# Optimization experiments

Hardware: AMD Instinct MI355X
Metric: run time of the kernel (lower is better)

The kernel has to match this reference:

```python
import jax, jax.numpy as jnp
import numpy as np

KEY_DIM = 512
VALUE_DIM = 128
CAPACITY = 500000
N_RETRIEVE = 16
LN_EPS = 1e-5
NORM_EPS = 1e-12


def _l2norm(x, axis=-1):
    # F.normalize: x / max(||x||, eps)
    n = jnp.sqrt(jnp.sum(x * x, axis=axis, keepdims=True))
    return x / jnp.maximum(n, NORM_EPS)


def setup_inputs() -> dict:
    key = jax.random.key(0)
    ks = jax.random.split(key, 5)
    s = 1.0 / np.sqrt(KEY_DIM)
    return {
        "query": jax.random.normal(ks[0], (1, KEY_DIM), jnp.float32),
        "W1": jax.random.normal(ks[1], (KEY_DIM, KEY_DIM), jnp.float32) * s,
        "b1": jnp.zeros((KEY_DIM,), jnp.float32),
        "W2": jax.random.normal(ks[2], (KEY_DIM, KEY_DIM), jnp.float32) * s,
        "b2": jnp.zeros((KEY_DIM,), jnp.float32),
        "gamma": jnp.ones((KEY_DIM,), jnp.float32),
        "beta": jnp.zeros((KEY_DIM,), jnp.float32),
        "keys": jax.random.normal(ks[3], (CAPACITY, KEY_DIM), jnp.float32),
        "values": jax.random.normal(ks[4], (CAPACITY, VALUE_DIM), jnp.float32),
    }


def reference(query, W1, b1, W2, b2, gamma, beta, keys, values):
    # read path detaches the query before projecting
    q = jax.lax.stop_gradient(query)                      # [1, D]
    h = jax.nn.silu(q @ W1.T + b1) @ W2.T + b2            # key_proj
    mu = jnp.mean(h, axis=-1, keepdims=True)
    var = jnp.var(h, axis=-1, keepdims=True)              # biased, like torch LN
    ln = (h - mu) / jnp.sqrt(var + LN_EPS) * gamma + beta
    qn = _l2norm(ln)[0]                                   # [D]
    kn = _l2norm(keys, axis=-1)                           # [N, D]
    sim = kn @ qn                                         # [N] cosine similarity
    top_sim, top_idx = jax.lax.top_k(sim, N_RETRIEVE)     # [k]
    attn = jax.nn.softmax(top_sim, axis=0)                # [k]
    vals = values[top_idx]                                # [k, V] gather
    out = attn @ vals                                     # [V] weighted sum
    return out
```

## Files before the change

### kernel.cpp

```cpp
#include <hip/hip_runtime.h>
#include <hip/hip_bf16.h>
#include <float.h>
#include <math.h>

#define KEY_DIM   512
#define VALUE_DIM 128
#define CAPACITY  500000
#define NRET      16

#define NBLKD     512
#define NBLKV     256
#define NBLKT     (NBLKD + NBLKV)
#define NSD       70
#define NDROWS    (NBLKD * NSD * 8)
#define ROFF      NDROWS
#define NVROWS    (CAPACITY - NDROWS)
#define VSWEEP    (NBLKV * 4 * 4)
#define RING      3

#define AS3 __attribute__((address_space(3)))
#define AS1 __attribute__((address_space(1)))

__device__ __forceinline__ float wave_sum(float x) {
#pragma unroll
    for (int s = 32; s > 0; s >>= 1) x += __shfl_xor(x, s);
    return x;
}

template <bool SILU>
__global__ __launch_bounds__(256) void matvec512(
        const float* __restrict__ W, const float* __restrict__ x,
        const float* __restrict__ b, float* __restrict__ y) {
    const int wid  = threadIdx.x >> 6;
    const int lane = threadIdx.x & 63;
    const int r = blockIdx.x * 4 + wid;

    const float4* Wr = (const float4*)(W + (size_t)r * KEY_DIM);
    const float4* xv = (const float4*)x;

    float4 w0 = Wr[lane], w1 = Wr[lane + 64];
    float4 x0 = xv[lane], x1 = xv[lane + 64];

    float dot = w0.x * x0.x + w0.y * x0.y + w0.z * x0.z + w0.w * x0.w
              + w1.x * x1.x + w1.y * x1.y + w1.z * x1.z + w1.w * x1.w;
    dot = wave_sum(dot);

    if (lane == 0) {
        float v = dot + b[r];
        if (SILU) v = v / (1.0f + expf(-v));
        y[r] = v;
    }
}

__global__ __launch_bounds__(512) void ln_l2norm(
        const float* __restrict__ h, const float* __restrict__ gamma,
        const float* __restrict__ beta, float* __restrict__ qn) {
    __shared__ float s1[8], s2[8];
    const int t = threadIdx.x;
    const int wid = t >> 6, lane = t & 63;

    float x = h[t];
    float a = x, bb = x * x;
#pragma unroll
    for (int s = 32; s > 0; s >>= 1) { a += __shfl_xor(a, s); bb += __shfl_xor(bb, s); }
    if (lane == 0) { s1[wid] = a; s2[wid] = bb; }
    __syncthreads();

    float suma = 0.f, sumb = 0.f;
#pragma unroll
    for (int i = 0; i < 8; ++i) { suma += s1[i]; sumb += s2[i]; }
    float mu  = suma * (1.0f / KEY_DIM);
    float var = sumb * (1.0f / KEY_DIM) - mu * mu;
    float ln  = (x - mu) / sqrtf(var + 1e-5f) * gamma[t] + beta[t];

    float c = wave_sum(ln * ln);
    __syncthreads();
    if (lane == 0) s1[wid] = c;
    __syncthreads();
    float ss = 0.f;
#pragma unroll
    for (int i = 0; i < 8; ++i) ss += s1[i];
    float n = fmaxf(sqrtf(ss), 1e-12f);
    qn[t] = ln / n;
}

__global__ __launch_bounds__(256) void sim_hybrid(
        const float* __restrict__ keys, const float* __restrict__ qn,
        float* __restrict__ cand_v, int* __restrict__ cand_i) {
    __shared__ float kl[RING][8][KEY_DIM];
    __shared__ float bv[64];
    __shared__ int   bi[64];

    const int tid  = threadIdx.x;
    const int w    = tid >> 6;
    const int lane = tid & 63;
    const int bid  = blockIdx.x;
    const int r3   = bid % 3;

    float v[16]; int id[16];
#pragma unroll
    for (int j = 0; j < 16; ++j) { v[j] = -FLT_MAX; id[j] = 0x7fffffff; }

    if (r3 < 2) {
        const int d    = (bid / 3) * 2 + r3;
        const int m    = lane & 31;
        const int rsel = lane >> 5;
        const int s0   = (d * 7919) % NSD;

        float4 qr[4];
        {
            const float4* q4 = (const float4*)qn;
#pragma unroll
            for (int j = 0; j < 4; ++j) qr[j] = q4[4 * m + j];
        }
        int srcoff0, srcoff1;
        {
            int p0 = lane,      g0 = p0 >> 2, sl0 = p0 & 3;
            int p1 = 64 + lane, g1 = p1 >> 2, sl1 = p1 & 3;
            srcoff0 = (4 * g0 + ((sl0 - (g0 >> 1)) & 3)) * 16;
            srcoff1 = (4 * g1 + ((sl1 - (g1 >> 1)) & 3)) * 16;
        }
        int roff[4];
#pragma unroll
        for (int j = 0; j < 4; ++j) roff[j] = (4 * m + ((j + (m >> 1)) & 3)) * 16;

        auto stage = [&](int G, int slot) {
#pragma unroll
            for (int i = 0; i < 4; ++i) {
                const int rl = 2 * w + (i >> 1);
                const int h  = i & 1;
                const char* gp = (const char*)(keys + ((size_t)G * 8 + rl) * KEY_DIM)
                                 + (h ? srcoff1 : srcoff0);
                float* lp = &kl[slot][rl][h * 256];
                __builtin_amdgcn_global_load_lds((const AS1 float*)gp, (AS3 float*)lp,
                                                 16, 0, 0);
            }
        };
        auto compute = [&](int G, int slot) {
            const char* rowbase = (const char*)&kl[slot][2 * w + rsel][0];
            float dot = 0.f, ss = 0.f;
#pragma unroll
            for (int j = 0; j < 4; ++j) {
                float4 k = *(const float4*)(rowbase + roff[j]);
                float4 q = qr[j];
                dot += k.x * q.x + k.y * q.y + k.z * q.z + k.w * q.w;
                ss  += k.x * k.x + k.y * k.y + k.z * k.z + k.w * k.w;
            }
#pragma unroll
            for (int s = 16; s > 0; s >>= 1) {
                dot += __shfl_xor(dot, s);
                ss  += __shfl_xor(ss, s);
            }
            float sim = dot / fmaxf(sqrtf(ss), 1e-12f);
#pragma unroll
            for (int q = 0; q < 2; ++q) {
                float sq = __shfl(sim, q * 32);
                if (sq > v[15]) {
                    float cv = sq; int ci = G * 8 + 2 * w + q;
#pragma unroll
                    for (int jj = 0; jj < 16; ++jj) {
                        if (cv > v[jj]) {
                            float tv = v[jj]; int ti = id[jj];
                            v[jj] = cv; id[jj] = ci; cv = tv; ci = ti;
                        }
                    }
                }
            }
        };

        {
            int se = s0;
            stage(d + se * NBLKD, 0);
            se = (se + 1 >= NSD) ? 0 : se + 1;
            stage(d + se * NBLKD, 1);
        }
        int scur = s0;
        int spre = s0 + 2; if (spre >= NSD) spre -= NSD;

#pragma unroll 1
        for (int s = 0; s < NSD; ++s) {
            stage(d + spre * NBLKD, (s + 2) % 3);
            spre = (spre + 1 >= NSD) ? 0 : spre + 1;
            asm volatile("s_waitcnt vmcnt(8)" ::: "memory");
            __builtin_amdgcn_sched_barrier(0);
            compute(d + scur * NBLKD, s % 3);
            __builtin_amdgcn_sched_barrier(0);
            scur = (scur + 1 >= NSD) ? 0 : scur + 1;
        }
        asm volatile("s_waitcnt vmcnt(0)" ::: "memory");
    } else {
        const int gw = (bid / 3) * 4 + w;
        const float4* q4 = (const float4*)qn;
        float4 q0 = q4[lane], q1 = q4[lane + 64];

#pragma unroll 1
        for (int base = gw * 4; base < NVROWS; base += VSWEEP) {
            float4 ka[4], kb[4];
#pragma unroll
            for (int j = 0; j < 4; ++j) {
                const float4* kp = (const float4*)(keys + (size_t)(ROFF + base + j) * KEY_DIM);
                ka[j] = kp[lane];
                kb[j] = kp[lane + 64];
            }
            float dot[4], ss[4];
#pragma unroll
            for (int j = 0; j < 4; ++j) {
                dot[j] = ka[j].x * q0.x + ka[j].y * q0.y + ka[j].z * q0.z + ka[j].w * q0.w
                       + kb[j].x * q1.x + kb[j].y * q1.y + kb[j].z * q1.z + kb[j].w * q1.w;
                ss[j]  = ka[j].x * ka[j].x + ka[j].y * ka[j].y + ka[j].z * ka[j].z + ka[j].w * ka[j].w
                       + kb[j].x * kb[j].x + kb[j].y * kb[j].y + kb[j].z * kb[j].z + kb[j].w * kb[j].w;
            }
#pragma unroll
            for (int s = 32; s > 0; s >>= 1) {
#pragma unroll
                for (int j = 0; j < 4; ++j) {
                    dot[j] += __shfl_xor(dot[j], s);
                    ss[j]  += __shfl_xor(ss[j], s);
                }
            }
#pragma unroll
            for (int j = 0; j < 4; ++j) {
                float sim = dot[j] / fmaxf(sqrtf(ss[j]), 1e-12f);
                if (sim > v[15]) {
                    float cv = sim; int ci = ROFF + base + j;
#pragma unroll
                    for (int jj = 0; jj < 16; ++jj) {
                        if (cv > v[jj]) {
                            float tv = v[jj]; int ti = id[jj];
                            v[jj] = cv; id[jj] = ci; cv = tv; ci = ti;
                        }
                    }
                }
            }
        }
    }

    if (lane == 0) {
#pragma unroll
        for (int j = 0; j < 16; ++j) { bv[w * 16 + j] = v[j]; bi[w * 16 + j] = id[j]; }
    }
    __syncthreads();
    if (w == 0) {
        const int cidx = (r3 < 2) ? ((bid / 3) * 2 + r3) : (NBLKD + bid / 3);
        float lv = bv[lane]; int li = bi[lane];
        for (int rr = 0; rr < NRET; ++rr) {
            float mv = lv; int mi = li;
#pragma unroll
            for (int s = 32; s > 0; s >>= 1) {
                float ov = __shfl_xor(mv, s); int oi = __shfl_xor(mi, s);
                if (ov > mv || (ov == mv && oi < mi)) { mv = ov; mi = oi; }
            }
            if (lane == 0) {
                cand_v[cidx * NRET + rr] = mv;
                cand_i[cidx * NRET + rr] = mi;
            }
            if (lv == mv && li == mi) { lv = -FLT_MAX; li = 0x7fffffff; }
        }
    }
}

__global__ __launch_bounds__(256) void merge_out(
        const float* __restrict__ cand_v, const int* __restrict__ cand_i,
        const float* __restrict__ values, float* __restrict__ out) {
    const int tid  = threadIdx.x;
    const int wid  = tid >> 6;
    const int lane = tid & 63;
    const int M4 = (NBLKT * NRET) / 4;

    float v[16]; int id[16];
#pragma unroll
    for (int j = 0; j < 16; ++j) { v[j] = -FLT_MAX; id[j] = 0x7fffffff; }

    const float4* cv4 = (const float4*)cand_v;
    const int4*   ci4 = (const int4*)cand_i;
    for (int c = tid; c < M4; c += 256) {
        float4 cv = cv4[c]; int4 ci = ci4[c];
        float cvs[4] = {cv.x, cv.y, cv.z, cv.w};
        int   cis[4] = {ci.x, ci.y, ci.z, ci.w};
#pragma unroll
        for (int u = 0; u < 4; ++u) {
            float cu = cvs[u]; int iu = cis[u];
            if (cu > v[15]) {
#pragma unroll
                for (int j = 0; j < 16; ++j) {
                    if (cu > v[j]) {
                        float tv = v[j]; int ti = id[j];
                        v[j] = cu; id[j] = iu; cu = tv; iu = ti;
                    }
                }
            }
        }
    }

    __shared__ float sv[64];
    __shared__ int   si[64];
    for (int rr = 0; rr < NRET; ++rr) {
        float mv = v[0]; int mi = id[0];
#pragma unroll
        for (int s = 32; s > 0; s >>= 1) {
            float ov = __shfl_xor(mv, s); int oi = __shfl_xor(mi, s);
            if (ov > mv || (ov == mv && oi < mi)) { mv = ov; mi = oi; }
        }
        if (v[0] == mv && id[0] == mi) {
#pragma unroll
            for (int j = 0; j < 15; ++j) { v[j] = v[j + 1]; id[j] = id[j + 1]; }
            v[15] = -FLT_MAX; id[15] = 0x7fffffff;
        }
        if (lane == 0) { sv[wid * 16 + rr] = mv; si[wid * 16 + rr] = mi; }
    }
    __syncthreads();

    if (wid == 0) {
        float lv = sv[lane]; int li = si[lane];
        float sel_v = -FLT_MAX; int sel_i = 0;
        for (int rr = 0; rr < NRET; ++rr) {
            float mv = lv; int mi = li;
#pragma unroll
            for (int s = 32; s > 0; s >>= 1) {
                float ov = __shfl_xor(mv, s); int oi = __shfl_xor(mi, s);
                if (ov > mv || (ov == mv && oi < mi)) { mv = ov; mi = oi; }
            }
            if (lv == mv && li == mi) { lv = -FLT_MAX; li = 0x7fffffff; }
            if (lane == rr) { sel_v = mv; sel_i = mi; }
        }

        float m0 = __shfl(sel_v, 0);
        float e = (lane < NRET) ? expf(sel_v - m0) : 0.0f;
        float denom = wave_sum(e);

        float acc0 = 0.f, acc1 = 0.f;
        for (int rr = 0; rr < NRET; ++rr) {
            float ar = __shfl(e, rr) / denom;
            int   ir = __shfl(sel_i, rr);
            const float* vr = values + (size_t)ir * VALUE_DIM;
            acc0 += ar * vr[lane];
            acc1 += ar * vr[lane + 64];
        }
        out[lane]      = acc0;
        out[lane + 64] = acc1;
    }
}

extern "C" void kernel_launch(void* const* d_in, const int* in_sizes, int n_in,
                              void* d_out, int out_size, void* d_ws, size_t ws_size,
                              hipStream_t stream) {
    const float* query  = (const float*)d_in[0];
    const float* W1     = (const float*)d_in[1];
    const float* b1     = (const float*)d_in[2];
    const float* W2     = (const float*)d_in[3];
    const float* b2     = (const float*)d_in[4];
    const float* gamma  = (const float*)d_in[5];
    const float* beta   = (const float*)d_in[6];
    const float* keys   = (const float*)d_in[7];
    const float* values = (const float*)d_in[8];
    float* out = (float*)d_out;

    float* ws = (float*)d_ws;
    float* h1     = ws;
    float* h2     = ws + 512;
    float* qn     = ws + 1024;
    float* cand_v = ws + 2048;
    int*   cand_i = (int*)(ws + 2048 + NBLKT * NRET);

    matvec512<true ><<<128, 256, 0, stream>>>(W1, query, b1, h1);
    matvec512<false><<<128, 256, 0, stream>>>(W2, h1, b2, h2);
    ln_l2norm<<<1, 512, 0, stream>>>(h2, gamma, beta, qn);
    sim_hybrid<<<NBLKT, 256, 0, stream>>>(keys, qn, cand_v, cand_i);
    merge_out<<<1, 256, 0, stream>>>(cand_v, cand_i, values, out);
}
```

Measured before the change: 313.1 us.

## Split DMA and direct-load work inside each block instead of across blocks

Replaces the block-level split with a split inside each block: every block now runs three waves on the LDS-DMA path and one wave on direct vector loads. The LDS-DMA path stages 6 rows per step and grows its ring from 3 to 4 slots, so three stages stay in flight. The row split is rebalanced to about 400k rows on the DMA path and the rest on direct loads. This aims to balance memory traffic across CUs and deepen prefetch. The risk is that a block now finishes only when its slowest wave does, so a mismatch between the two paths leaves waves idle.

```diff
diff --git a/kernel.cpp b/kernel.cpp
--- a/kernel.cpp
+++ b/kernel.cpp
@@ -8,15 +8,12 @@
 #define CAPACITY  500000
 #define NRET      16
 
-#define NBLKD     512
-#define NBLKV     256
-#define NBLKT     (NBLKD + NBLKV)
-#define NSD       70
-#define NDROWS    (NBLKD * NSD * 8)
-#define ROFF      NDROWS
-#define NVROWS    (CAPACITY - NDROWS)
-#define VSWEEP    (NBLKV * 4 * 4)
-#define RING      3
+#define NBLKS     768
+#define RING      4
+#define NSD       87
+#define DROWS     (NBLKS * 6 * NSD)
+#define VOFF      DROWS
+#define VSWEEP    (NBLKS * 4)
 
 #define AS3 __attribute__((address_space(3)))
 #define AS1 __attribute__((address_space(1)))
@@ -84,10 +81,10 @@
     qn[t] = ln / n;
 }
 
-__global__ __launch_bounds__(256) void sim_hybrid(
+__global__ __launch_bounds__(256) void sim_split(
         const float* __restrict__ keys, const float* __restrict__ qn,
         float* __restrict__ cand_v, int* __restrict__ cand_i) {
-    __shared__ float kl[RING][8][KEY_DIM];
+    __shared__ float kl[RING][6][KEY_DIM];
     __shared__ float bv[64];
     __shared__ int   bi[64];
 
@@ -95,17 +92,15 @@
     const int w    = tid >> 6;
     const int lane = tid & 63;
     const int bid  = blockIdx.x;
-    const int r3   = bid % 3;
 
     float v[16]; int id[16];
 #pragma unroll
     for (int j = 0; j < 16; ++j) { v[j] = -FLT_MAX; id[j] = 0x7fffffff; }
 
-    if (r3 < 2) {
-        const int d    = (bid / 3) * 2 + r3;
+    if (w < 3) {
         const int m    = lane & 31;
         const int rsel = lane >> 5;
-        const int s0   = (d * 7919) % NSD;
+        const int s0   = (bid * 7919) % NSD;
 
         float4 qr[4];
         {
@@ -124,19 +119,19 @@
 #pragma unroll
         for (int j = 0; j < 4; ++j) roff[j] = (4 * m + ((j + (m >> 1)) & 3)) * 16;
 
-        auto stage = [&](int G, int slot) {
+        auto stage = [&](int T, int slot) {
 #pragma unroll
             for (int i = 0; i < 4; ++i) {
                 const int rl = 2 * w + (i >> 1);
                 const int h  = i & 1;
-                const char* gp = (const char*)(keys + ((size_t)G * 8 + rl) * KEY_DIM)
+                const char* gp = (const char*)(keys + ((size_t)T * 6 + rl) * KEY_DIM)
                                  + (h ? srcoff1 : srcoff0);
                 float* lp = &kl[slot][rl][h * 256];
                 __builtin_amdgcn_global_load_lds((const AS1 float*)gp, (AS3 float*)lp,
                                                  16, 0, 0);
             }
         };
-        auto compute = [&](int G, int slot) {
+        auto compute = [&](int T, int slot) {
             const char* rowbase = (const char*)&kl[slot][2 * w + rsel][0];
             float dot = 0.f, ss = 0.f;
 #pragma unroll
@@ -153,10 +148,10 @@
             }
             float sim = dot / fmaxf(sqrtf(ss), 1e-12f);
 #pragma unroll
-            for (int q = 0; q < 2; ++q) {
-                float sq = __shfl(sim, q * 32);
+            for (int qq = 0; qq < 2; ++qq) {
+                float sq = __shfl(sim, qq * 32);
                 if (sq > v[15]) {
-                    float cv = sq; int ci = G * 8 + 2 * w + q;
+                    float cv = sq; int ci = T * 6 + 2 * w + qq;
 #pragma unroll
                     for (int jj = 0; jj < 16; ++jj) {
                         if (cv > v[jj]) {
@@ -170,35 +165,36 @@
 
         {
             int se = s0;
-            stage(d + se * NBLKD, 0);
+            stage(bid + se * NBLKS, 0);
             se = (se + 1 >= NSD) ? 0 : se + 1;
-            stage(d + se * NBLKD, 1);
+            stage(bid + se * NBLKS, 1);
+            se = (se + 1 >= NSD) ? 0 : se + 1;
+            stage(bid + se * NBLKS, 2);
         }
         int scur = s0;
-        int spre = s0 + 2; if (spre >= NSD) spre -= NSD;
+        int spre = s0 + 3; if (spre >= NSD) spre -= NSD;
 
 #pragma unroll 1
         for (int s = 0; s < NSD; ++s) {
-            stage(d + spre * NBLKD, (s + 2) % 3);
+            stage(bid + spre * NBLKS, (s + 3) & 3);
             spre = (spre + 1 >= NSD) ? 0 : spre + 1;
-            asm volatile("s_waitcnt vmcnt(8)" ::: "memory");
+            asm volatile("s_waitcnt vmcnt(12)" ::: "memory");
             __builtin_amdgcn_sched_barrier(0);
-            compute(d + scur * NBLKD, s % 3);
+            compute(bid + scur * NBLKS, s & 3);
             __builtin_amdgcn_sched_barrier(0);
             scur = (scur + 1 >= NSD) ? 0 : scur + 1;
         }
         asm volatile("s_waitcnt vmcnt(0)" ::: "memory");
     } else {
-        const int gw = (bid / 3) * 4 + w;
         const float4* q4 = (const float4*)qn;
         float4 q0 = q4[lane], q1 = q4[lane + 64];
 
 #pragma unroll 1
-        for (int base = gw * 4; base < NVROWS; base += VSWEEP) {
+        for (int base = VOFF + bid * 4; base < CAPACITY; base += VSWEEP) {
             float4 ka[4], kb[4];
 #pragma unroll
             for (int j = 0; j < 4; ++j) {
-                const float4* kp = (const float4*)(keys + (size_t)(ROFF + base + j) * KEY_DIM);
+                const float4* kp = (const float4*)(keys + (size_t)(base + j) * KEY_DIM);
                 ka[j] = kp[lane];
                 kb[j] = kp[lane + 64];
             }
@@ -222,7 +218,7 @@
             for (int j = 0; j < 4; ++j) {
                 float sim = dot[j] / fmaxf(sqrtf(ss[j]), 1e-12f);
                 if (sim > v[15]) {
-                    float cv = sim; int ci = ROFF + base + j;
+                    float cv = sim; int ci = base + j;
 #pragma unroll
                     for (int jj = 0; jj < 16; ++jj) {
                         if (cv > v[jj]) {
@@ -241,7 +237,6 @@
     }
     __syncthreads();
     if (w == 0) {
-        const int cidx = (r3 < 2) ? ((bid / 3) * 2 + r3) : (NBLKD + bid / 3);
         float lv = bv[lane]; int li = bi[lane];
         for (int rr = 0; rr < NRET; ++rr) {
             float mv = lv; int mi = li;
@@ -251,8 +246,8 @@
                 if (ov > mv || (ov == mv && oi < mi)) { mv = ov; mi = oi; }
             }
             if (lane == 0) {
-                cand_v[cidx * NRET + rr] = mv;
-                cand_i[cidx * NRET + rr] = mi;
+                cand_v[bid * NRET + rr] = mv;
+                cand_i[bid * NRET + rr] = mi;
             }
             if (lv == mv && li == mi) { lv = -FLT_MAX; li = 0x7fffffff; }
         }
@@ -265,7 +260,7 @@
     const int tid  = threadIdx.x;
     const int wid  = tid >> 6;
     const int lane = tid & 63;
-    const int M4 = (NBLKT * NRET) / 4;
+    const int M4 = (NBLKS * NRET) / 4;
 
     float v[16]; int id[16];
 #pragma unroll
@@ -360,11 +355,11 @@
     float* h2     = ws + 512;
     float* qn     = ws + 1024;
     float* cand_v = ws + 2048;
-    int*   cand_i = (int*)(ws + 2048 + NBLKT * NRET);
+    int*   cand_i = (int*)(ws + 2048 + NBLKS * NRET);
 
     matvec512<true ><<<128, 256, 0, stream>>>(W1, query, b1, h1);
     matvec512<false><<<128, 256, 0, stream>>>(W2, h1, b2, h2);
     ln_l2norm<<<1, 512, 0, stream>>>(h2, gamma, beta, qn);
-    sim_hybrid<<<NBLKT, 256, 0, stream>>>(keys, qn, cand_v, cand_i);
+    sim_split<<<NBLKS, 256, 0, stream>>>(keys, qn, cand_v, cand_i);
     merge_out<<<1, 256, 0, stream>>>(cand_v, cand_i, values, out);
 }
```

Result: faster. 272.5 us (-13.0%).
